# Optimization experiments

Hardware: AMD Instinct MI355X
Metric: run time of the kernel (lower is better)

Reference implementation:

```python
import jax, jax.numpy as jnp
import numpy as np

N_NODES = 50000
NEG_SLOPE = 0.2  # PyG GATConv default leaky_relu slope


def gat_layer(x, edge_index, W, a_src, a_dst, bias, heads, out_dim, concat):
    """PyG-style GATConv with self-loops.
    x: [N, F_in]; edge_index: [2, E]; W: [F_in, heads*out_dim];
    a_src, a_dst: [heads, out_dim]; bias: [heads*out_dim] or [out_dim].
    """
    N = x.shape[0]
    # add self loops (PyG default add_self_loops=True)
    ar = jnp.arange(N, dtype=edge_index.dtype)
    ei = jnp.concatenate([edge_index, jnp.stack([ar, ar])], axis=1)
    src, dst = ei[0], ei[1]

    h = (x @ W).reshape(N, heads, out_dim)            # [N, H, F]
    alpha_src = jnp.einsum('nhf,hf->nh', h, a_src)    # [N, H]
    alpha_dst = jnp.einsum('nhf,hf->nh', h, a_dst)

    e = alpha_src[src] + alpha_dst[dst]               # [E, H]
    e = jax.nn.leaky_relu(e, NEG_SLOPE)

    # segment softmax over incoming edges of each dst node
    m = jax.ops.segment_max(e, dst, num_segments=N)   # [N, H]
    ex = jnp.exp(e - m[dst])
    denom = jax.ops.segment_sum(ex, dst, num_segments=N)
    alpha = ex / denom[dst]                           # [E, H]

    msg = alpha[:, :, None] * h[src]                  # [E, H, F]
    out = jax.ops.segment_sum(msg, dst, num_segments=N)  # [N, H, F]

    if concat:
        out = out.reshape(N, heads * out_dim)
    else:
        out = out.mean(axis=1)
    return out + bias


def setup_inputs() -> dict:
    key = jax.random.key(0)
    ks = jax.random.split(key, 10)
    node_dim, hidden = 128, 64
    x = jax.random.normal(ks[0], (N_NODES, node_dim), dtype=jnp.float32)
    edge_index = jax.random.randint(ks[1], (2, 600000), 0, N_NODES, dtype=jnp.int64)
    s1 = 1.0 / np.sqrt(node_dim)
    s2 = 1.0 / np.sqrt(2 * hidden)
    return {
        'x': x,
        'edge_index': edge_index,
        'W1': jax.random.normal(ks[2], (node_dim, 2 * hidden), dtype=jnp.float32) * s1,
        'a_src1': jax.random.normal(ks[3], (2, hidden), dtype=jnp.float32) * s1,
        'a_dst1': jax.random.normal(ks[4], (2, hidden), dtype=jnp.float32) * s1,
        'b1': jnp.zeros((2 * hidden,), dtype=jnp.float32),
        'W2': jax.random.normal(ks[5], (2 * hidden, hidden), dtype=jnp.float32) * s2,
        'a_src2': jax.random.normal(ks[6], (1, hidden), dtype=jnp.float32) * s2,
        'a_dst2': jax.random.normal(ks[7], (1, hidden), dtype=jnp.float32) * s2,
        'b2': jnp.zeros((hidden,), dtype=jnp.float32),
    }


def reference(x, edge_index, W1, a_src1, a_dst1, b1, W2, a_src2, a_dst2, b2):
    h = gat_layer(x, edge_index, W1, a_src1, a_dst1, b1, heads=2, out_dim=64, concat=True)
    h = jax.nn.elu(h)
    out = gat_layer(h, edge_index, W2, a_src2, a_dst2, b2, heads=1, out_dim=64, concat=False)
    return out
```

## Files before the change

### kernel.cpp

```cpp
#include <hip/hip_runtime.h>
#include <hip/hip_bf16.h>


#define LRELU_SLOPE 0.2f
#define CAP 64

typedef __bf16 v8bf __attribute__((ext_vector_type(8)));
typedef float f32x4 __attribute__((ext_vector_type(4)));


__device__ __forceinline__ unsigned short bf16r(float x) {
    unsigned u = __float_as_uint(x);
    return (unsigned short)((u + 0x7fff + ((u >> 16) & 1)) >> 16);
}
__device__ __forceinline__ unsigned pbf(float a, float b) {
    return (unsigned)bf16r(a) | ((unsigned)bf16r(b) << 16);
}
__device__ __forceinline__ float bflo(unsigned u) { return __uint_as_float(u << 16); }
__device__ __forceinline__ float bfhi(unsigned u) { return __uint_as_float(u & 0xffff0000u); }

__device__ __forceinline__ v8bf ldfrag(const char* base, int row, int kb) {
    uint4 u = *(const uint4*)(base + row * 256 + (kb ^ ((row & 7) << 4)));
    return __builtin_bit_cast(v8bf, u);
}
__device__ __forceinline__ v8bf ldwt(const unsigned short* wt, int n, int kb) {
    uint4 u = *(const uint4*)((const char*)wt + n * 256 + kb);
    return __builtin_bit_cast(v8bf, u);
}


__global__ void prep_kernel(const float* __restrict__ W1, const float* __restrict__ W2,
                            unsigned short* __restrict__ wt1,
                            unsigned short* __restrict__ wt2,
                            int* __restrict__ cnt, unsigned short* __restrict__ srcs,
                            int N) {
    int b = blockIdx.x, tid = threadIdx.x;
    if (b < 3) {
        int id = b * 256 + tid;
        int n = id >> 2, kq = id & 3;
        if (n < 128) {
            #pragma unroll 8
            for (int j = 0; j < 32; j++) {
                int k = kq * 32 + j;
                wt1[n * 128 + k] = bf16r(W1[k * 128 + n]);
            }
        } else if (n < 192) {
            int n2 = n - 128;
            #pragma unroll 8
            for (int j = 0; j < 32; j++) {
                int k = kq * 32 + j;
                wt2[n2 * 128 + k] = bf16r(W2[k * 64 + n2]);
            }
        }
    } else {
        int i = (b - 3) * 256 + tid;
        if (i < N) {
            cnt[i] = 1;
            srcs[(size_t)i * CAP] = (unsigned short)i;
        }
    }
}


__global__ __launch_bounds__(256) void sg_kernel(const float* __restrict__ X,
        const unsigned short* __restrict__ wt, const float* __restrict__ asw,
        const float* __restrict__ adw, unsigned short* __restrict__ hb,
        float* __restrict__ as_out, float* __restrict__ ad_out, int M, int GS,
        const int* __restrict__ ei, int E, int* __restrict__ cnt,
        unsigned short* __restrict__ srcs) {
    __shared__ uint4 xs4[1024];
    __shared__ float aps[4][64], apd[4][64];
    int t = threadIdx.x;

    if (blockIdx.x < GS) {
        int t8 = (blockIdx.x * 256 + t) * 8;
        if (t8 + 7 < E) {
            int4 s0 = *(const int4*)(ei + t8);
            int4 s1 = *(const int4*)(ei + t8 + 4);
            int4 d0 = *(const int4*)(ei + E + t8);
            int4 d1 = *(const int4*)(ei + E + t8 + 4);
            int p0 = atomicAdd(&cnt[d0.x], 1);
            int p1 = atomicAdd(&cnt[d0.y], 1);
            int p2 = atomicAdd(&cnt[d0.z], 1);
            int p3 = atomicAdd(&cnt[d0.w], 1);
            int p4 = atomicAdd(&cnt[d1.x], 1);
            int p5 = atomicAdd(&cnt[d1.y], 1);
            int p6 = atomicAdd(&cnt[d1.z], 1);
            int p7 = atomicAdd(&cnt[d1.w], 1);
            if (p0 < CAP) __builtin_nontemporal_store((unsigned short)s0.x, &srcs[(size_t)d0.x * CAP + p0]);
            if (p1 < CAP) __builtin_nontemporal_store((unsigned short)s0.y, &srcs[(size_t)d0.y * CAP + p1]);
            if (p2 < CAP) __builtin_nontemporal_store((unsigned short)s0.z, &srcs[(size_t)d0.z * CAP + p2]);
            if (p3 < CAP) __builtin_nontemporal_store((unsigned short)s0.w, &srcs[(size_t)d0.w * CAP + p3]);
            if (p4 < CAP) __builtin_nontemporal_store((unsigned short)s1.x, &srcs[(size_t)d1.x * CAP + p4]);
            if (p5 < CAP) __builtin_nontemporal_store((unsigned short)s1.y, &srcs[(size_t)d1.y * CAP + p5]);
            if (p6 < CAP) __builtin_nontemporal_store((unsigned short)s1.z, &srcs[(size_t)d1.z * CAP + p6]);
            if (p7 < CAP) __builtin_nontemporal_store((unsigned short)s1.w, &srcs[(size_t)d1.w * CAP + p7]);
        } else {
            for (int j = 0; j < 8; j++) {
                int e = t8 + j;
                if (e < E) {
                    int d = ei[E + e];
                    int pos = atomicAdd(&cnt[d], 1);
                    if (pos < CAP) srcs[(size_t)d * CAP + pos] = (unsigned short)ei[e];
                }
            }
        }
        return;
    }

    char* xs = (char*)xs4;
    int row0 = (blockIdx.x - GS) * 64;
    int lane = t & 63, w = t >> 6;

    {
        int kq = t & 31;
        for (int m = t >> 5; m < 64; m += 8) {
            int gr = row0 + m;
            float4 v = make_float4(0.f, 0.f, 0.f, 0.f);
            if (gr < M) v = *(const float4*)(X + (size_t)gr * 128 + kq * 4);
            *(uint2*)(xs + m * 256 + ((kq * 8) ^ ((m & 7) << 4))) =
                make_uint2(pbf(v.x, v.y), pbf(v.z, v.w));
        }
    }
    __syncthreads();

    int l15 = lane & 15, lhi = lane >> 4;
    f32x4 acc[4][2];
    #pragma unroll
    for (int rt = 0; rt < 4; rt++) { acc[rt][0] = (f32x4)(0.f); acc[rt][1] = (f32x4)(0.f); }

    #pragma unroll
    for (int ks = 0; ks < 4; ks++) {
        int kb = ks * 64 + lhi * 16;
        v8bf b0 = ldwt(wt, w * 32 + l15, kb);
        v8bf b1 = ldwt(wt, w * 32 + 16 + l15, kb);
        #pragma unroll
        for (int rt = 0; rt < 4; rt++) {
            v8bf a = ldfrag(xs, rt * 16 + l15, kb);
            acc[rt][0] = __builtin_amdgcn_mfma_f32_16x16x32_bf16(a, b0, acc[rt][0], 0, 0, 0);
            acc[rt][1] = __builtin_amdgcn_mfma_f32_16x16x32_bf16(a, b1, acc[rt][1], 0, 0, 0);
        }
    }

    float asv0 = asw[w * 32 + l15],      adv0 = adw[w * 32 + l15];
    float asv1 = asw[w * 32 + 16 + l15], adv1 = adw[w * 32 + 16 + l15];
    #pragma unroll
    for (int rt = 0; rt < 4; rt++) {
        #pragma unroll
        for (int r = 0; r < 4; r++) {
            int m = rt * 16 + lhi * 4 + r;
            int gr = row0 + m;
            float v0 = acc[rt][0][r], v1 = acc[rt][1][r];
            if (gr < M) {
                hb[(size_t)gr * 128 + w * 32 + l15]      = bf16r(v0);
                hb[(size_t)gr * 128 + w * 32 + 16 + l15] = bf16r(v1);
            }
            float ps = v0 * asv0 + v1 * asv1;
            float pd = v0 * adv0 + v1 * adv1;
            #pragma unroll
            for (int o = 1; o < 16; o <<= 1) { ps += __shfl_xor(ps, o); pd += __shfl_xor(pd, o); }
            if (l15 == 0) { aps[w][m] = ps; apd[w][m] = pd; }
        }
    }
    __syncthreads();
    if (t < 128) {
        int m = t & 63, hd = t >> 6;
        int gr = row0 + m;
        if (gr < M) {
            as_out[gr * 2 + hd] = aps[hd * 2][m] + aps[hd * 2 + 1][m];
            ad_out[gr * 2 + hd] = apd[hd * 2][m] + apd[hd * 2 + 1][m];
        }
    }
}


__global__ __launch_bounds__(256) void gemm2_kernel(const unsigned short* __restrict__ X,
        const unsigned short* __restrict__ wt, const float* __restrict__ asw,
        const float* __restrict__ adw, unsigned short* __restrict__ hb2,
        float* __restrict__ as_out, float* __restrict__ ad_out, int M) {
    __shared__ uint4 xs4[1024];
    __shared__ float aps[4][64], apd[4][64];
    char* xs = (char*)xs4;
    int t = threadIdx.x;
    int row0 = blockIdx.x * 64;
    int lane = t & 63, w = t >> 6;

    {
        int slot = t & 15;
        for (int m = t >> 4; m < 64; m += 16) {
            int gr = row0 + m;
            uint4 v = make_uint4(0, 0, 0, 0);
            if (gr < M) v = *(const uint4*)(X + (size_t)gr * 128 + slot * 8);
            *(uint4*)(xs + m * 256 + ((slot * 16) ^ ((m & 7) << 4))) = v;
        }
    }
    __syncthreads();

    int l15 = lane & 15, lhi = lane >> 4;
    f32x4 acc[4];
    #pragma unroll
    for (int rt = 0; rt < 4; rt++) acc[rt] = (f32x4)(0.f);

    #pragma unroll
    for (int ks = 0; ks < 4; ks++) {
        int kb = ks * 64 + lhi * 16;
        v8bf b0 = ldwt(wt, w * 16 + l15, kb);
        #pragma unroll
        for (int rt = 0; rt < 4; rt++) {
            v8bf a = ldfrag(xs, rt * 16 + l15, kb);
            acc[rt] = __builtin_amdgcn_mfma_f32_16x16x32_bf16(a, b0, acc[rt], 0, 0, 0);
        }
    }

    float asv = asw[w * 16 + l15], adv = adw[w * 16 + l15];
    #pragma unroll
    for (int rt = 0; rt < 4; rt++) {
        #pragma unroll
        for (int r = 0; r < 4; r++) {
            int m = rt * 16 + lhi * 4 + r;
            int gr = row0 + m;
            float v0 = acc[rt][r];
            if (gr < M) hb2[(size_t)gr * 64 + w * 16 + l15] = bf16r(v0);
            float ps = v0 * asv;
            float pd = v0 * adv;
            #pragma unroll
            for (int o = 1; o < 16; o <<= 1) { ps += __shfl_xor(ps, o); pd += __shfl_xor(pd, o); }
            if (l15 == 0) { aps[w][m] = ps; apd[w][m] = pd; }
        }
    }
    __syncthreads();
    if (t < 64) {
        int gr = row0 + t;
        if (gr < M) {
            as_out[gr] = aps[0][t] + aps[1][t] + aps[2][t] + aps[3][t];
            ad_out[gr] = apd[0][t] + apd[1][t] + apd[2][t] + apd[3][t];
        }
    }
}


__global__ __launch_bounds__(256) void agg1_kernel(const uint4* __restrict__ hb,
        const float2* __restrict__ asrc, const float2* __restrict__ adst,
        const int* __restrict__ cnt, const unsigned short* __restrict__ srcs,
        const float* __restrict__ bias, unsigned short* __restrict__ helu_b, int N) {
    int tid = threadIdx.x, wid = tid >> 6, lane = tid & 63;
    int n = blockIdx.x * 4 + wid;
    if (n >= N) return;
    int chunk = lane & 15;
    int slot  = lane >> 4;
    size_t start = (size_t)n * CAP;
    int deg = min(cnt[n], CAP);
    float2 ad = adst[n];

    float acc[8];
    #pragma unroll
    for (int k = 0; k < 8; k++) acc[k] = 0.f;
    float dsum0 = 0.f, dsum1 = 0.f;

    {
        int s = 0; float w0 = 0.f, w1 = 0.f;
        if (lane < deg) {
            s = srcs[start + lane];
            float2 av = asrc[s];
            float e0 = av.x + ad.x; e0 = (e0 >= 0.f) ? e0 : LRELU_SLOPE * e0;
            float e1 = av.y + ad.y; e1 = (e1 >= 0.f) ? e1 : LRELU_SLOPE * e1;
            w0 = __expf(e0); w1 = __expf(e1);
        }
        dsum0 += w0; dsum1 += w1;

        for (int j0 = 0; j0 < deg; j0 += 8) {
            int ea = j0 + slot, eb = j0 + 4 + slot;
            int sa = __shfl(s, ea), sb = __shfl(s, eb);
            float wa0 = __shfl(w0, ea), wa1 = __shfl(w1, ea);
            float wb0 = __shfl(w0, eb), wb1 = __shfl(w1, eb);
            float wa = (chunk >= 8) ? wa1 : wa0;
            float wb = (chunk >= 8) ? wb1 : wb0;
            uint4 ua = make_uint4(0, 0, 0, 0), ub = make_uint4(0, 0, 0, 0);
            if (ea < deg) ua = hb[(size_t)sa * 16 + chunk];
            if (eb < deg) ub = hb[(size_t)sb * 16 + chunk];
            acc[0] += wa * bflo(ua.x) + wb * bflo(ub.x);
            acc[1] += wa * bfhi(ua.x) + wb * bfhi(ub.x);
            acc[2] += wa * bflo(ua.y) + wb * bflo(ub.y);
            acc[3] += wa * bfhi(ua.y) + wb * bfhi(ub.y);
            acc[4] += wa * bflo(ua.z) + wb * bflo(ub.z);
            acc[5] += wa * bfhi(ua.z) + wb * bfhi(ub.z);
            acc[6] += wa * bflo(ua.w) + wb * bflo(ub.w);
            acc[7] += wa * bfhi(ua.w) + wb * bfhi(ub.w);
        }
    }

    #pragma unroll
    for (int k = 0; k < 8; k++) {
        acc[k] += __shfl_xor(acc[k], 16);
        acc[k] += __shfl_xor(acc[k], 32);
    }
    #pragma unroll
    for (int o = 1; o < 64; o <<= 1) {
        dsum0 += __shfl_xor(dsum0, o);
        dsum1 += __shfl_xor(dsum1, o);
    }
    if (slot == 0) {
        float inv = 1.f / ((chunk >= 8) ? dsum1 : dsum0);
        int f = chunk * 8;
        float q[8];
        #pragma unroll
        for (int k = 0; k < 8; k++) {
            q[k] = acc[k] * inv + bias[f + k];
            q[k] = (q[k] > 0.f) ? q[k] : __expf(q[k]) - 1.f;
        }
        *(uint4*)&helu_b[(size_t)n * 128 + f] = make_uint4(
            pbf(q[0], q[1]), pbf(q[2], q[3]), pbf(q[4], q[5]), pbf(q[6], q[7]));
    }
}


__global__ __launch_bounds__(256) void agg2_kernel(const uint4* __restrict__ hb2,
        const float* __restrict__ asrc, const float* __restrict__ adst,
        const int* __restrict__ cnt, const unsigned short* __restrict__ srcs,
        const float* __restrict__ bias, float* __restrict__ out, int N) {
    int tid = threadIdx.x, wid = tid >> 6, lane = tid & 63;
    int n = blockIdx.x * 4 + wid;
    if (n >= N) return;
    int chunk = lane & 7;
    int slot  = lane >> 3;
    size_t start = (size_t)n * CAP;
    int deg = min(cnt[n], CAP);
    float ad = adst[n];

    float acc[8];
    #pragma unroll
    for (int k = 0; k < 8; k++) acc[k] = 0.f;
    float dsum = 0.f;

    {
        int s = 0; float w = 0.f;
        if (lane < deg) {
            s = srcs[start + lane];
            float e = asrc[s] + ad;
            e = (e >= 0.f) ? e : LRELU_SLOPE * e;
            w = __expf(e);
        }
        dsum += w;

        for (int j0 = 0; j0 < deg; j0 += 16) {
            int ea = j0 + slot, eb = j0 + 8 + slot;
            int sa = __shfl(s, ea), sb = __shfl(s, eb);
            float wa = __shfl(w, ea), wb = __shfl(w, eb);
            uint4 ua = make_uint4(0, 0, 0, 0), ub = make_uint4(0, 0, 0, 0);
            if (ea < deg) ua = hb2[(size_t)sa * 8 + chunk];
            if (eb < deg) ub = hb2[(size_t)sb * 8 + chunk];
            acc[0] += wa * bflo(ua.x) + wb * bflo(ub.x);
            acc[1] += wa * bfhi(ua.x) + wb * bfhi(ub.x);
            acc[2] += wa * bflo(ua.y) + wb * bflo(ub.y);
            acc[3] += wa * bfhi(ua.y) + wb * bfhi(ub.y);
            acc[4] += wa * bflo(ua.z) + wb * bflo(ub.z);
            acc[5] += wa * bfhi(ua.z) + wb * bfhi(ub.z);
            acc[6] += wa * bflo(ua.w) + wb * bflo(ub.w);
            acc[7] += wa * bfhi(ua.w) + wb * bfhi(ub.w);
        }
    }

    #pragma unroll
    for (int k = 0; k < 8; k++) {
        acc[k] += __shfl_xor(acc[k], 8);
        acc[k] += __shfl_xor(acc[k], 16);
        acc[k] += __shfl_xor(acc[k], 32);
    }
    #pragma unroll
    for (int o = 1; o < 64; o <<= 1) dsum += __shfl_xor(dsum, o);
    if (slot == 0) {
        float inv = 1.f / dsum;
        int f = chunk * 8;
        float q[8];
        #pragma unroll
        for (int k = 0; k < 8; k++) q[k] = acc[k] * inv + bias[f + k];
        *(float4*)&out[(size_t)n * 64 + f]     = make_float4(q[0], q[1], q[2], q[3]);
        *(float4*)&out[(size_t)n * 64 + f + 4] = make_float4(q[4], q[5], q[6], q[7]);
    }
}


extern "C" void kernel_launch(void* const* d_in, const int* in_sizes, int n_in,
                              void* d_out, int out_size, void* d_ws, size_t ws_size,
                              hipStream_t stream) {
    const float* x    = (const float*)d_in[0];
    const int*   ei   = (const int*)d_in[1];
    const float* W1   = (const float*)d_in[2];
    const float* as1w = (const float*)d_in[3];
    const float* ad1w = (const float*)d_in[4];
    const float* b1   = (const float*)d_in[5];
    const float* W2   = (const float*)d_in[6];
    const float* as2w = (const float*)d_in[7];
    const float* ad2w = (const float*)d_in[8];
    const float* b2   = (const float*)d_in[9];
    float* out = (float*)d_out;

    const int N  = in_sizes[0] / 128;
    const int E  = in_sizes[1] / 2;

    char* base = (char*)d_ws;
    size_t off = 0;
    auto alloc = [&](size_t bytes) -> void* {
        void* p = base + off;
        off += (bytes + 255) & ~(size_t)255;
        return p;
    };
    unsigned short* hb1  = (unsigned short*)alloc((size_t)N * 128 * 2);
    unsigned short* hbel = (unsigned short*)alloc((size_t)N * 128 * 2);
    unsigned short* hb2  = (unsigned short*)alloc((size_t)N * 64 * 2);
    float* as1     = (float*)alloc((size_t)N * 2 * 4);
    float* ad1     = (float*)alloc((size_t)N * 2 * 4);
    float* as2     = (float*)alloc((size_t)N * 4);
    float* ad2     = (float*)alloc((size_t)N * 4);
    int*   cnt     = (int*)alloc((size_t)N * 4);
    unsigned short* srcs = (unsigned short*)alloc((size_t)N * CAP * 2);
    unsigned short* wt1 = (unsigned short*)alloc(128 * 128 * 2);
    unsigned short* wt2 = (unsigned short*)alloc(64 * 128 * 2);

    const int G1 = (N + 63) / 64;
    const int GS = (E / 8 + 255) / 256;

    prep_kernel<<<3 + (N + 255) / 256, 256, 0, stream>>>(W1, W2, wt1, wt2,
                                                         cnt, srcs, N);
    sg_kernel<<<GS + G1, 256, 0, stream>>>(x, wt1, as1w, ad1w, hb1, as1, ad1,
                                           N, GS, ei, E, cnt, srcs);
    agg1_kernel<<<(N + 3) / 4, 256, 0, stream>>>((const uint4*)hb1,
                                                 (const float2*)as1, (const float2*)ad1,
                                                 cnt, srcs, b1, hbel, N);
    gemm2_kernel<<<(N + 63) / 64, 256, 0, stream>>>(hbel, wt2, as2w, ad2w,
                                                    hb2, as2, ad2, N);
    agg2_kernel<<<(N + 3) / 4, 256, 0, stream>>>((const uint4*)hb2, as2, ad2,
                                                 cnt, srcs, b2, out, N);
}
```

Baseline: 130.0 us.

## Build CSR-like adjacency per destination range with shared-memory counters

Edge bucketing now gives each block a range of 256 destination nodes. Each block scans the whole edge list and uses shared-memory atomics for the edges that land in its range, instead of global atomics on a counter array. Counter and self-loop initialisation move from the prep kernel into these blocks, so the prep launch shrinks to three blocks. The catch is that every bucketing block reads all E destination indices (about 196 blocks each reading 2.4MB), which trades global atomic contention for redundant reads served mostly from cache. The stored counts are now clamped to CAP.

```diff
diff --git a/kernel.cpp b/kernel.cpp
--- a/kernel.cpp
+++ b/kernel.cpp
@@ -31,32 +31,21 @@
 
 __global__ void prep_kernel(const float* __restrict__ W1, const float* __restrict__ W2,
                             unsigned short* __restrict__ wt1,
-                            unsigned short* __restrict__ wt2,
-                            int* __restrict__ cnt, unsigned short* __restrict__ srcs,
-                            int N) {
-    int b = blockIdx.x, tid = threadIdx.x;
-    if (b < 3) {
-        int id = b * 256 + tid;
-        int n = id >> 2, kq = id & 3;
-        if (n < 128) {
-            #pragma unroll 8
-            for (int j = 0; j < 32; j++) {
-                int k = kq * 32 + j;
-                wt1[n * 128 + k] = bf16r(W1[k * 128 + n]);
-            }
-        } else if (n < 192) {
-            int n2 = n - 128;
-            #pragma unroll 8
-            for (int j = 0; j < 32; j++) {
-                int k = kq * 32 + j;
-                wt2[n2 * 128 + k] = bf16r(W2[k * 64 + n2]);
-            }
-        }
-    } else {
-        int i = (b - 3) * 256 + tid;
-        if (i < N) {
-            cnt[i] = 1;
-            srcs[(size_t)i * CAP] = (unsigned short)i;
+                            unsigned short* __restrict__ wt2) {
+    int id = blockIdx.x * 256 + threadIdx.x;
+    int n = id >> 2, kq = id & 3;
+    if (n < 128) {
+        #pragma unroll 8
+        for (int j = 0; j < 32; j++) {
+            int k = kq * 32 + j;
+            wt1[n * 128 + k] = bf16r(W1[k * 128 + n]);
+        }
+    } else if (n < 192) {
+        int n2 = n - 128;
+        #pragma unroll 8
+        for (int j = 0; j < 32; j++) {
+            int k = kq * 32 + j;
+            wt2[n2 * 128 + k] = bf16r(W2[k * 64 + n2]);
         }
     }
 }
@@ -68,46 +57,39 @@
         float* __restrict__ as_out, float* __restrict__ ad_out, int M, int GS,
         const int* __restrict__ ei, int E, int* __restrict__ cnt,
         unsigned short* __restrict__ srcs) {
+    int t = threadIdx.x;
+
+    if (blockIdx.x < GS) {
+        __shared__ int lcnt[256];
+        int base = blockIdx.x * 256;
+        int n = base + t;
+        bool valid = n < M;
+        lcnt[t] = 1;
+        if (valid) srcs[(size_t)n * CAP] = (unsigned short)n;
+        __syncthreads();
+
+        const int* __restrict__ dsts = ei + E;
+        for (int e0 = t * 8; e0 < E; e0 += 256 * 8) {
+            int4 d0 = *(const int4*)(dsts + e0);
+            int4 d1 = *(const int4*)(dsts + e0 + 4);
+            int dd[8] = {d0.x, d0.y, d0.z, d0.w, d1.x, d1.y, d1.z, d1.w};
+            #pragma unroll
+            for (int j = 0; j < 8; j++) {
+                unsigned rel = (unsigned)(dd[j] - base);
+                if (rel < 256u) {
+                    int pos = atomicAdd(&lcnt[rel], 1);
+                    if (pos < CAP)
+                        srcs[(size_t)dd[j] * CAP + pos] = (unsigned short)ei[e0 + j];
+                }
+            }
+        }
+        __syncthreads();
+        if (valid) cnt[n] = min(lcnt[t], CAP);
+        return;
+    }
+
     __shared__ uint4 xs4[1024];
     __shared__ float aps[4][64], apd[4][64];
-    int t = threadIdx.x;
-
-    if (blockIdx.x < GS) {
-        int t8 = (blockIdx.x * 256 + t) * 8;
-        if (t8 + 7 < E) {
-            int4 s0 = *(const int4*)(ei + t8);
-            int4 s1 = *(const int4*)(ei + t8 + 4);
-            int4 d0 = *(const int4*)(ei + E + t8);
-            int4 d1 = *(const int4*)(ei + E + t8 + 4);
-            int p0 = atomicAdd(&cnt[d0.x], 1);
-            int p1 = atomicAdd(&cnt[d0.y], 1);
-            int p2 = atomicAdd(&cnt[d0.z], 1);
-            int p3 = atomicAdd(&cnt[d0.w], 1);
-            int p4 = atomicAdd(&cnt[d1.x], 1);
-            int p5 = atomicAdd(&cnt[d1.y], 1);
-            int p6 = atomicAdd(&cnt[d1.z], 1);
-            int p7 = atomicAdd(&cnt[d1.w], 1);
-            if (p0 < CAP) __builtin_nontemporal_store((unsigned short)s0.x, &srcs[(size_t)d0.x * CAP + p0]);
-            if (p1 < CAP) __builtin_nontemporal_store((unsigned short)s0.y, &srcs[(size_t)d0.y * CAP + p1]);
-            if (p2 < CAP) __builtin_nontemporal_store((unsigned short)s0.z, &srcs[(size_t)d0.z * CAP + p2]);
-            if (p3 < CAP) __builtin_nontemporal_store((unsigned short)s0.w, &srcs[(size_t)d0.w * CAP + p3]);
-            if (p4 < CAP) __builtin_nontemporal_store((unsigned short)s1.x, &srcs[(size_t)d1.x * CAP + p4]);
-            if (p5 < CAP) __builtin_nontemporal_store((unsigned short)s1.y, &srcs[(size_t)d1.y * CAP + p5]);
-            if (p6 < CAP) __builtin_nontemporal_store((unsigned short)s1.z, &srcs[(size_t)d1.z * CAP + p6]);
-            if (p7 < CAP) __builtin_nontemporal_store((unsigned short)s1.w, &srcs[(size_t)d1.w * CAP + p7]);
-        } else {
-            for (int j = 0; j < 8; j++) {
-                int e = t8 + j;
-                if (e < E) {
-                    int d = ei[E + e];
-                    int pos = atomicAdd(&cnt[d], 1);
-                    if (pos < CAP) srcs[(size_t)d * CAP + pos] = (unsigned short)ei[e];
-                }
-            }
-        }
-        return;
-    }
-
     char* xs = (char*)xs4;
     int row0 = (blockIdx.x - GS) * 64;
     int lane = t & 63, w = t >> 6;
@@ -418,10 +400,9 @@
     unsigned short* wt2 = (unsigned short*)alloc(64 * 128 * 2);
 
     const int G1 = (N + 63) / 64;
-    const int GS = (E / 8 + 255) / 256;
-
-    prep_kernel<<<3 + (N + 255) / 256, 256, 0, stream>>>(W1, W2, wt1, wt2,
-                                                         cnt, srcs, N);
+    const int GS = (N + 255) / 256;
+
+    prep_kernel<<<3, 256, 0, stream>>>(W1, W2, wt1, wt2);
     sg_kernel<<<GS + G1, 256, 0, stream>>>(x, wt1, as1w, ad1w, hb1, as1, ad1,
                                            N, GS, ei, E, cnt, srcs);
     agg1_kernel<<<(N + 3) / 4, 256, 0, stream>>>((const uint4*)hb1,
```

Result: slower. 325.6 us (+150.5%).
